# Optimization experiments

Hardware: AMD Instinct MI355X
Metric: run time of the kernel (lower is better)

## Reference

```python
import jax, jax.numpy as jnp
import numpy as np

B, T, I, H, OUT, L = 256, 1200, 16, 128, 1, 2


def _lstm_layer(x, W_ih, W_hh, b_ih, b_hh):
    # x: [B, T, Din]; W_ih: [4H, Din]; W_hh: [4H, H]
    # Precompute input contribution for all timesteps (one big GEMM),
    # then scan only the recurrent part.
    pre = jnp.einsum('btd,gd->btg', x, W_ih) + b_ih + b_hh  # [B, T, 4H]
    pre = jnp.swapaxes(pre, 0, 1)  # [T, B, 4H]
    h0 = jnp.zeros((x.shape[0], W_hh.shape[1]), dtype=x.dtype)
    c0 = jnp.zeros_like(h0)

    def step(carry, p_t):
        h, c = carry
        g = p_t + h @ W_hh.T  # [B, 4H]
        i, f, gg, o = jnp.split(g, 4, axis=-1)  # torch gate order: i, f, g, o
        i = jax.nn.sigmoid(i)
        f = jax.nn.sigmoid(f)
        gg = jnp.tanh(gg)
        o = jax.nn.sigmoid(o)
        c = f * c + i * gg
        h = o * jnp.tanh(c)
        return (h, c), h

    (_, _), hs = jax.lax.scan(step, (h0, c0), pre)  # hs: [T, B, H]
    return jnp.swapaxes(hs, 0, 1)  # [B, T, H]


def setup_inputs() -> dict:
    key = jax.random.key(0)
    ks = jax.random.split(key, 12)
    s = 0.08  # small init scale to keep gates unsaturated
    inp = {
        'x': jax.random.normal(ks[0], (B, T, I), dtype=jnp.float32),
        'W_ih0': jax.random.normal(ks[1], (4 * H, I), dtype=jnp.float32) * s,
        'W_hh0': jax.random.normal(ks[2], (4 * H, H), dtype=jnp.float32) * s,
        'b_ih0': jax.random.normal(ks[3], (4 * H,), dtype=jnp.float32) * s,
        'b_hh0': jax.random.normal(ks[4], (4 * H,), dtype=jnp.float32) * s,
        'W_ih1': jax.random.normal(ks[5], (4 * H, H), dtype=jnp.float32) * s,
        'W_hh1': jax.random.normal(ks[6], (4 * H, H), dtype=jnp.float32) * s,
        'b_ih1': jax.random.normal(ks[7], (4 * H,), dtype=jnp.float32) * s,
        'b_hh1': jax.random.normal(ks[8], (4 * H,), dtype=jnp.float32) * s,
        'W_lin': jax.random.normal(ks[9], (OUT, H), dtype=jnp.float32) * s,
        'b_lin': jax.random.normal(ks[10], (OUT,), dtype=jnp.float32) * s,
    }
    return inp


def reference(x, W_ih0, W_hh0, b_ih0, b_hh0, W_ih1, W_hh1, b_ih1, b_hh1, W_lin, b_lin):
    h1 = _lstm_layer(x, W_ih0, W_hh0, b_ih0, b_hh0)   # [B, T, H]
    h2 = _lstm_layer(h1, W_ih1, W_hh1, b_ih1, b_hh1)  # [B, T, H]
    out = jax.nn.relu(h2)
    out = jnp.einsum('bth,oh->bto', out, W_lin) + b_lin  # [B, T, OUT]
    return out.reshape(-1, 12)  # [B*T*OUT/12, 12]
```

## Files before the change

kernel.cpp:

```cpp
#include <hip/hip_runtime.h>
#include <hip/hip_fp16.h>

#define B_ 256
#define T_ 1200
#define I_ 16
#define H_ 128

typedef __attribute__((ext_vector_type(2))) _Float16 h2;
typedef __attribute__((ext_vector_type(8))) _Float16 f16x8;

#if __has_builtin(__builtin_amdgcn_fdot2)
__device__ __forceinline__ float fdot2(h2 a, h2 b, float c) {
  return __builtin_amdgcn_fdot2(a, b, c, false);
}
#else
__device__ __forceinline__ float fdot2(h2 a, h2 b, float c) {
  return fmaf((float)a.x, (float)b.x, fmaf((float)a.y, (float)b.y, c));
}
#endif

__device__ __forceinline__ float qsum(float x) {
  x += __int_as_float(__builtin_amdgcn_update_dpp(0, __float_as_int(x), 0xB1, 0xF, 0xF, true));
  x += __int_as_float(__builtin_amdgcn_update_dpp(0, __float_as_int(x), 0x4E, 0xF, 0xF, true));
  return x;
}

__device__ __forceinline__ float sigm(float x) {
  return __builtin_amdgcn_rcpf(1.f + __expf(-x));
}
__device__ __forceinline__ float tanh_(float x) {
  return 1.f - 2.f * __builtin_amdgcn_rcpf(1.f + __expf(2.f * x));
}

#define DECL16(p) h2 p##0,p##1,p##2,p##3,p##4,p##5,p##6,p##7,p##8,p##9,p##10,p##11,p##12,p##13,p##14,p##15;

#define LOADROW(p, src) { \
  const float4 v0_ = *(const float4*)((src) + 0); \
  const float4 v1_ = *(const float4*)((src) + 4); \
  const float4 v2_ = *(const float4*)((src) + 8); \
  const float4 v3_ = *(const float4*)((src) + 12); \
  const float4 v4_ = *(const float4*)((src) + 16); \
  const float4 v5_ = *(const float4*)((src) + 20); \
  const float4 v6_ = *(const float4*)((src) + 24); \
  const float4 v7_ = *(const float4*)((src) + 28); \
  p##0 .x=(_Float16)v0_.x;  p##0 .y=(_Float16)v0_.y;  p##1 .x=(_Float16)v0_.z;  p##1 .y=(_Float16)v0_.w; \
  p##2 .x=(_Float16)v1_.x;  p##2 .y=(_Float16)v1_.y;  p##3 .x=(_Float16)v1_.z;  p##3 .y=(_Float16)v1_.w; \
  p##4 .x=(_Float16)v2_.x;  p##4 .y=(_Float16)v2_.y;  p##5 .x=(_Float16)v2_.z;  p##5 .y=(_Float16)v2_.w; \
  p##6 .x=(_Float16)v3_.x;  p##6 .y=(_Float16)v3_.y;  p##7 .x=(_Float16)v3_.z;  p##7 .y=(_Float16)v3_.w; \
  p##8 .x=(_Float16)v4_.x;  p##8 .y=(_Float16)v4_.y;  p##9 .x=(_Float16)v4_.z;  p##9 .y=(_Float16)v4_.w; \
  p##10 .x=(_Float16)v5_.x; p##10 .y=(_Float16)v5_.y; p##11 .x=(_Float16)v5_.z; p##11 .y=(_Float16)v5_.w; \
  p##12 .x=(_Float16)v6_.x; p##12 .y=(_Float16)v6_.y; p##13 .x=(_Float16)v6_.z; p##13 .y=(_Float16)v6_.w; \
  p##14 .x=(_Float16)v7_.x; p##14 .y=(_Float16)v7_.y; p##15 .x=(_Float16)v7_.z; p##15 .y=(_Float16)v7_.w; }

#define H2AT(f, a, b) ({ h2 t_; t_.x = (f)[a]; t_.y = (f)[b]; t_; })

#define GDOT(mat, k0, k1, k2, k3, f) \
  a0 = fdot2(mat##_0_##k0, H2AT(f,0,1), a0); \
  a0 = fdot2(mat##_0_##k1, H2AT(f,2,3), a0); \
  a0 = fdot2(mat##_0_##k2, H2AT(f,4,5), a0); \
  a0 = fdot2(mat##_0_##k3, H2AT(f,6,7), a0); \
  a1 = fdot2(mat##_1_##k0, H2AT(f,0,1), a1); \
  a1 = fdot2(mat##_1_##k1, H2AT(f,2,3), a1); \
  a1 = fdot2(mat##_1_##k2, H2AT(f,4,5), a1); \
  a1 = fdot2(mat##_1_##k3, H2AT(f,6,7), a1); \
  a2 = fdot2(mat##_2_##k0, H2AT(f,0,1), a2); \
  a2 = fdot2(mat##_2_##k1, H2AT(f,2,3), a2); \
  a2 = fdot2(mat##_2_##k2, H2AT(f,4,5), a2); \
  a2 = fdot2(mat##_2_##k3, H2AT(f,6,7), a2); \
  a3 = fdot2(mat##_3_##k0, H2AT(f,0,1), a3); \
  a3 = fdot2(mat##_3_##k1, H2AT(f,2,3), a3); \
  a3 = fdot2(mat##_3_##k2, H2AT(f,4,5), a3); \
  a3 = fdot2(mat##_3_##k3, H2AT(f,6,7), a3);

#define MATDOT(mat, base) { \
  { const f16x8 f_ = *(const f16x8*)((base) + 0);  GDOT(mat, 0, 1, 2, 3,  f_) } \
  { const f16x8 f_ = *(const f16x8*)((base) + 8);  GDOT(mat, 4, 5, 6, 7,  f_) } \
  { const f16x8 f_ = *(const f16x8*)((base) + 16); GDOT(mat, 8, 9, 10,11, f_) } \
  { const f16x8 f_ = *(const f16x8*)((base) + 24); GDOT(mat, 12,13,14,15, f_) } }

__global__ __launch_bounds__(512)
__attribute__((amdgpu_waves_per_eu(2, 2)))
void lstm_fused(
    const float* __restrict__ xin,
    const float* __restrict__ Wih0, const float* __restrict__ Whh0,
    const float* __restrict__ bih0, const float* __restrict__ bhh0,
    const float* __restrict__ Wih1, const float* __restrict__ Whh1,
    const float* __restrict__ bih1, const float* __restrict__ bhh1,
    const float* __restrict__ Wlin, const float* __restrict__ blin,
    float* __restrict__ out)
{
  __shared__ __align__(16) __half buf0[2][H_];
  __shared__ __align__(16) __half buf1[2][H_];
  __shared__ __align__(16) float red[2][8];

  const int tid = threadIdx.x;
  const int c = tid & 3;
  const int j = tid >> 2;
  const int b = blockIdx.x;
  const int wv = tid >> 6;

  DECL16(w0_0_) DECL16(w0_1_) DECL16(w0_2_) DECL16(w0_3_)
  DECL16(wi_0_) DECL16(wi_1_) DECL16(wi_2_) DECL16(wi_3_)
  DECL16(wh_0_) DECL16(wh_1_) DECL16(wh_2_) DECL16(wh_3_)

  const int co = c * 32;
  LOADROW(w0_0_, Whh0 + (size_t)(0 * H_ + j) * H_ + co)
  LOADROW(w0_1_, Whh0 + (size_t)(1 * H_ + j) * H_ + co)
  LOADROW(w0_2_, Whh0 + (size_t)(2 * H_ + j) * H_ + co)
  LOADROW(w0_3_, Whh0 + (size_t)(3 * H_ + j) * H_ + co)
  LOADROW(wi_0_, Wih1 + (size_t)(0 * H_ + j) * H_ + co)
  LOADROW(wi_1_, Wih1 + (size_t)(1 * H_ + j) * H_ + co)
  LOADROW(wi_2_, Wih1 + (size_t)(2 * H_ + j) * H_ + co)
  LOADROW(wi_3_, Wih1 + (size_t)(3 * H_ + j) * H_ + co)
  LOADROW(wh_0_, Whh1 + (size_t)(0 * H_ + j) * H_ + co)
  LOADROW(wh_1_, Whh1 + (size_t)(1 * H_ + j) * H_ + co)
  LOADROW(wh_2_, Whh1 + (size_t)(2 * H_ + j) * H_ + co)
  LOADROW(wh_3_, Whh1 + (size_t)(3 * H_ + j) * H_ + co)

  h2 wx00, wx01, wx10, wx11, wx20, wx21, wx30, wx31;
  {
    const float4 v0 = *(const float4*)(Wih0 + (size_t)(0 * H_ + j) * I_ + 4 * c);
    const float4 v1 = *(const float4*)(Wih0 + (size_t)(1 * H_ + j) * I_ + 4 * c);
    const float4 v2 = *(const float4*)(Wih0 + (size_t)(2 * H_ + j) * I_ + 4 * c);
    const float4 v3 = *(const float4*)(Wih0 + (size_t)(3 * H_ + j) * I_ + 4 * c);
    wx00.x=(_Float16)v0.x; wx00.y=(_Float16)v0.y; wx01.x=(_Float16)v0.z; wx01.y=(_Float16)v0.w;
    wx10.x=(_Float16)v1.x; wx10.y=(_Float16)v1.y; wx11.x=(_Float16)v1.z; wx11.y=(_Float16)v1.w;
    wx20.x=(_Float16)v2.x; wx20.y=(_Float16)v2.y; wx21.x=(_Float16)v2.z; wx21.y=(_Float16)v2.w;
    wx30.x=(_Float16)v3.x; wx30.y=(_Float16)v3.y; wx31.x=(_Float16)v3.z; wx31.y=(_Float16)v3.w;
  }
  const float bs0_0 = bih0[0*H_+j] + bhh0[0*H_+j];
  const float bs0_1 = bih0[1*H_+j] + bhh0[1*H_+j];
  const float bs0_2 = bih0[2*H_+j] + bhh0[2*H_+j];
  const float bs0_3 = bih0[3*H_+j] + bhh0[3*H_+j];
  const float bs1_0 = bih1[0*H_+j] + bhh1[0*H_+j];
  const float bs1_1 = bih1[1*H_+j] + bhh1[1*H_+j];
  const float bs1_2 = bih1[2*H_+j] + bhh1[2*H_+j];
  const float bs1_3 = bih1[3*H_+j] + bhh1[3*H_+j];

  const float wl4 = Wlin[j] * 0.25f;
  const float bl = blin[0];

  if (tid < H_) {
    buf0[0][tid] = __float2half(0.f);
    buf1[0][tid] = __float2half(0.f);
  }
  float cst0 = 0.f, cst1 = 0.f;
  const float* xp = xin + (size_t)b * T_ * I_ + 4 * c;
  float* op = out + (size_t)b * T_;
  float4 xv_next = *(const float4*)xp;
  __syncthreads();

#pragma unroll 2
  for (int t = 0; t < T_; ++t) {
    const int rb = t & 1;
    const float4 xv = xv_next;
    xp += I_;
    if (t + 1 < T_) xv_next = *(const float4*)xp;
    float a0 = 0.f, a1 = 0.f, a2 = 0.f, a3 = 0.f;
    MATDOT(w0, &buf0[rb][co])
    {
      h2 xa, xb;
      xa.x = (_Float16)xv.x; xa.y = (_Float16)xv.y;
      xb.x = (_Float16)xv.z; xb.y = (_Float16)xv.w;
      a0 = fdot2(wx00, xa, fdot2(wx01, xb, a0));
      a1 = fdot2(wx10, xa, fdot2(wx11, xb, a1));
      a2 = fdot2(wx20, xa, fdot2(wx21, xb, a2));
      a3 = fdot2(wx30, xa, fdot2(wx31, xb, a3));
      const float g0 = qsum(a0) + bs0_0;
      const float g1 = qsum(a1) + bs0_1;
      const float g2 = qsum(a2) + bs0_2;
      const float g3 = qsum(a3) + bs0_3;
      const float ig = sigm(g0), fg = sigm(g1), gg = tanh_(g2), og = sigm(g3);
      cst0 = fg * cst0 + ig * gg;
      const float h0v = og * tanh_(cst0);
      if (c == 0) buf0[rb ^ 1][j] = __float2half(h0v);
    }
    __syncthreads();
    a0 = 0.f; a1 = 0.f; a2 = 0.f; a3 = 0.f;
    MATDOT(wi, &buf0[rb ^ 1][co])
    MATDOT(wh, &buf1[rb][co])
    const float g0 = qsum(a0) + bs1_0;
    const float g1 = qsum(a1) + bs1_1;
    const float g2 = qsum(a2) + bs1_2;
    const float g3 = qsum(a3) + bs1_3;
    const float ig = sigm(g0), fg = sigm(g1), gg = tanh_(g2), og = sigm(g3);
    cst1 = fg * cst1 + ig * gg;
    const float h1v = og * tanh_(cst1);
    if (c == 0) buf1[rb ^ 1][j] = __float2half(h1v);
    float val = fmaxf(h1v, 0.f) * wl4;
    val += __shfl_xor(val, 1);
    val += __shfl_xor(val, 2);
    val += __shfl_xor(val, 4);
    val += __shfl_xor(val, 8);
    val += __shfl_xor(val, 16);
    val += __shfl_xor(val, 32);
    if ((tid & 63) == 0) red[rb][wv] = val;
    __syncthreads();
    if (tid == ((t & 7) << 6)) {
      const float4 r0 = *(const float4*)(&red[rb][0]);
      const float4 r1 = *(const float4*)(&red[rb][4]);
      op[t] = bl + r0.x + r0.y + r0.z + r0.w + r1.x + r1.y + r1.z + r1.w;
    }
  }
}

extern "C" void kernel_launch(void* const* d_in, const int* in_sizes, int n_in,
                              void* d_out, int out_size, void* d_ws, size_t ws_size,
                              hipStream_t stream) {
  lstm_fused<<<B_, 512, 0, stream>>>(
      (const float*)d_in[0],
      (const float*)d_in[1], (const float*)d_in[2],
      (const float*)d_in[3], (const float*)d_in[4],
      (const float*)d_in[5], (const float*)d_in[6],
      (const float*)d_in[7], (const float*)d_in[8],
      (const float*)d_in[9], (const float*)d_in[10],
      (float*)d_out);
}
```

Measured before the change: 2.086 ms.

## Split each hidden unit across 8 lanes with 1024-thread blocks

Doubles the threads per block from 512 to 1024, so each hidden unit's dot product is split across 8 lanes instead of 4. Each lane now holds half as many fp16 weights in registers and does half the fdot2 work per step. The per-step reduction gains an extra ds_swizzle stage, and the final output reduction now combines 16 wave partials instead of 8. This shortens the serial per-timestep critical path, but makes each block-wide barrier more expensive and removes the waves_per_eu hint.

New measurement: 3.962 ms. 1.9x slower.

```diff
diff --git a/kernel.cpp b/kernel.cpp
--- a/kernel.cpp
+++ b/kernel.cpp
@@ -19,9 +19,10 @@
 }
 #endif
 
-__device__ __forceinline__ float qsum(float x) {
+__device__ __forceinline__ float osum(float x) {
   x += __int_as_float(__builtin_amdgcn_update_dpp(0, __float_as_int(x), 0xB1, 0xF, 0xF, true));
   x += __int_as_float(__builtin_amdgcn_update_dpp(0, __float_as_int(x), 0x4E, 0xF, 0xF, true));
+  x += __int_as_float(__builtin_amdgcn_ds_swizzle(__float_as_int(x), 0x101F));
   return x;
 }
 
@@ -32,25 +33,17 @@
   return 1.f - 2.f * __builtin_amdgcn_rcpf(1.f + __expf(2.f * x));
 }
 
-#define DECL16(p) h2 p##0,p##1,p##2,p##3,p##4,p##5,p##6,p##7,p##8,p##9,p##10,p##11,p##12,p##13,p##14,p##15;
-
-#define LOADROW(p, src) { \
+#define DECL8(p) h2 p##0,p##1,p##2,p##3,p##4,p##5,p##6,p##7;
+
+#define LOADROW8(p, src) { \
   const float4 v0_ = *(const float4*)((src) + 0); \
   const float4 v1_ = *(const float4*)((src) + 4); \
   const float4 v2_ = *(const float4*)((src) + 8); \
   const float4 v3_ = *(const float4*)((src) + 12); \
-  const float4 v4_ = *(const float4*)((src) + 16); \
-  const float4 v5_ = *(const float4*)((src) + 20); \
-  const float4 v6_ = *(const float4*)((src) + 24); \
-  const float4 v7_ = *(const float4*)((src) + 28); \
-  p##0 .x=(_Float16)v0_.x;  p##0 .y=(_Float16)v0_.y;  p##1 .x=(_Float16)v0_.z;  p##1 .y=(_Float16)v0_.w; \
-  p##2 .x=(_Float16)v1_.x;  p##2 .y=(_Float16)v1_.y;  p##3 .x=(_Float16)v1_.z;  p##3 .y=(_Float16)v1_.w; \
-  p##4 .x=(_Float16)v2_.x;  p##4 .y=(_Float16)v2_.y;  p##5 .x=(_Float16)v2_.z;  p##5 .y=(_Float16)v2_.w; \
-  p##6 .x=(_Float16)v3_.x;  p##6 .y=(_Float16)v3_.y;  p##7 .x=(_Float16)v3_.z;  p##7 .y=(_Float16)v3_.w; \
-  p##8 .x=(_Float16)v4_.x;  p##8 .y=(_Float16)v4_.y;  p##9 .x=(_Float16)v4_.z;  p##9 .y=(_Float16)v4_.w; \
-  p##10 .x=(_Float16)v5_.x; p##10 .y=(_Float16)v5_.y; p##11 .x=(_Float16)v5_.z; p##11 .y=(_Float16)v5_.w; \
-  p##12 .x=(_Float16)v6_.x; p##12 .y=(_Float16)v6_.y; p##13 .x=(_Float16)v6_.z; p##13 .y=(_Float16)v6_.w; \
-  p##14 .x=(_Float16)v7_.x; p##14 .y=(_Float16)v7_.y; p##15 .x=(_Float16)v7_.z; p##15 .y=(_Float16)v7_.w; }
+  p##0 .x=(_Float16)v0_.x; p##0 .y=(_Float16)v0_.y; p##1 .x=(_Float16)v0_.z; p##1 .y=(_Float16)v0_.w; \
+  p##2 .x=(_Float16)v1_.x; p##2 .y=(_Float16)v1_.y; p##3 .x=(_Float16)v1_.z; p##3 .y=(_Float16)v1_.w; \
+  p##4 .x=(_Float16)v2_.x; p##4 .y=(_Float16)v2_.y; p##5 .x=(_Float16)v2_.z; p##5 .y=(_Float16)v2_.w; \
+  p##6 .x=(_Float16)v3_.x; p##6 .y=(_Float16)v3_.y; p##7 .x=(_Float16)v3_.z; p##7 .y=(_Float16)v3_.w; }
 
 #define H2AT(f, a, b) ({ h2 t_; t_.x = (f)[a]; t_.y = (f)[b]; t_; })
 
@@ -72,15 +65,11 @@
   a3 = fdot2(mat##_3_##k2, H2AT(f,4,5), a3); \
   a3 = fdot2(mat##_3_##k3, H2AT(f,6,7), a3);
 
-#define MATDOT(mat, base) { \
-  { const f16x8 f_ = *(const f16x8*)((base) + 0);  GDOT(mat, 0, 1, 2, 3,  f_) } \
-  { const f16x8 f_ = *(const f16x8*)((base) + 8);  GDOT(mat, 4, 5, 6, 7,  f_) } \
-  { const f16x8 f_ = *(const f16x8*)((base) + 16); GDOT(mat, 8, 9, 10,11, f_) } \
-  { const f16x8 f_ = *(const f16x8*)((base) + 24); GDOT(mat, 12,13,14,15, f_) } }
-
-__global__ __launch_bounds__(512)
-__attribute__((amdgpu_waves_per_eu(2, 2)))
-void lstm_fused(
+#define MATDOT8(mat, base) { \
+  { const f16x8 f_ = *(const f16x8*)((base) + 0); GDOT(mat, 0, 1, 2, 3, f_) } \
+  { const f16x8 f_ = *(const f16x8*)((base) + 8); GDOT(mat, 4, 5, 6, 7, f_) } }
+
+__global__ __launch_bounds__(1024) void lstm_fused(
     const float* __restrict__ xin,
     const float* __restrict__ Wih0, const float* __restrict__ Whh0,
     const float* __restrict__ bih0, const float* __restrict__ bhh0,
@@ -91,42 +80,42 @@
 {
   __shared__ __align__(16) __half buf0[2][H_];
   __shared__ __align__(16) __half buf1[2][H_];
-  __shared__ __align__(16) float red[2][8];
+  __shared__ __align__(16) float red[2][16];
 
   const int tid = threadIdx.x;
-  const int c = tid & 3;
-  const int j = tid >> 2;
+  const int o = tid & 7;
+  const int j = tid >> 3;
   const int b = blockIdx.x;
   const int wv = tid >> 6;
 
-  DECL16(w0_0_) DECL16(w0_1_) DECL16(w0_2_) DECL16(w0_3_)
-  DECL16(wi_0_) DECL16(wi_1_) DECL16(wi_2_) DECL16(wi_3_)
-  DECL16(wh_0_) DECL16(wh_1_) DECL16(wh_2_) DECL16(wh_3_)
-
-  const int co = c * 32;
-  LOADROW(w0_0_, Whh0 + (size_t)(0 * H_ + j) * H_ + co)
-  LOADROW(w0_1_, Whh0 + (size_t)(1 * H_ + j) * H_ + co)
-  LOADROW(w0_2_, Whh0 + (size_t)(2 * H_ + j) * H_ + co)
-  LOADROW(w0_3_, Whh0 + (size_t)(3 * H_ + j) * H_ + co)
-  LOADROW(wi_0_, Wih1 + (size_t)(0 * H_ + j) * H_ + co)
-  LOADROW(wi_1_, Wih1 + (size_t)(1 * H_ + j) * H_ + co)
-  LOADROW(wi_2_, Wih1 + (size_t)(2 * H_ + j) * H_ + co)
-  LOADROW(wi_3_, Wih1 + (size_t)(3 * H_ + j) * H_ + co)
-  LOADROW(wh_0_, Whh1 + (size_t)(0 * H_ + j) * H_ + co)
-  LOADROW(wh_1_, Whh1 + (size_t)(1 * H_ + j) * H_ + co)
-  LOADROW(wh_2_, Whh1 + (size_t)(2 * H_ + j) * H_ + co)
-  LOADROW(wh_3_, Whh1 + (size_t)(3 * H_ + j) * H_ + co)
-
-  h2 wx00, wx01, wx10, wx11, wx20, wx21, wx30, wx31;
+  DECL8(w0_0_) DECL8(w0_1_) DECL8(w0_2_) DECL8(w0_3_)
+  DECL8(wi_0_) DECL8(wi_1_) DECL8(wi_2_) DECL8(wi_3_)
+  DECL8(wh_0_) DECL8(wh_1_) DECL8(wh_2_) DECL8(wh_3_)
+
+  const int co = o * 16;
+  LOADROW8(w0_0_, Whh0 + (size_t)(0 * H_ + j) * H_ + co)
+  LOADROW8(w0_1_, Whh0 + (size_t)(1 * H_ + j) * H_ + co)
+  LOADROW8(w0_2_, Whh0 + (size_t)(2 * H_ + j) * H_ + co)
+  LOADROW8(w0_3_, Whh0 + (size_t)(3 * H_ + j) * H_ + co)
+  LOADROW8(wi_0_, Wih1 + (size_t)(0 * H_ + j) * H_ + co)
+  LOADROW8(wi_1_, Wih1 + (size_t)(1 * H_ + j) * H_ + co)
+  LOADROW8(wi_2_, Wih1 + (size_t)(2 * H_ + j) * H_ + co)
+  LOADROW8(wi_3_, Wih1 + (size_t)(3 * H_ + j) * H_ + co)
+  LOADROW8(wh_0_, Whh1 + (size_t)(0 * H_ + j) * H_ + co)
+  LOADROW8(wh_1_, Whh1 + (size_t)(1 * H_ + j) * H_ + co)
+  LOADROW8(wh_2_, Whh1 + (size_t)(2 * H_ + j) * H_ + co)
+  LOADROW8(wh_3_, Whh1 + (size_t)(3 * H_ + j) * H_ + co)
+
+  h2 wx0, wx1, wx2, wx3;
   {
-    const float4 v0 = *(const float4*)(Wih0 + (size_t)(0 * H_ + j) * I_ + 4 * c);
-    const float4 v1 = *(const float4*)(Wih0 + (size_t)(1 * H_ + j) * I_ + 4 * c);
-    const float4 v2 = *(const float4*)(Wih0 + (size_t)(2 * H_ + j) * I_ + 4 * c);
-    const float4 v3 = *(const float4*)(Wih0 + (size_t)(3 * H_ + j) * I_ + 4 * c);
-    wx00.x=(_Float16)v0.x; wx00.y=(_Float16)v0.y; wx01.x=(_Float16)v0.z; wx01.y=(_Float16)v0.w;
-    wx10.x=(_Float16)v1.x; wx10.y=(_Float16)v1.y; wx11.x=(_Float16)v1.z; wx11.y=(_Float16)v1.w;
-    wx20.x=(_Float16)v2.x; wx20.y=(_Float16)v2.y; wx21.x=(_Float16)v2.z; wx21.y=(_Float16)v2.w;
-    wx30.x=(_Float16)v3.x; wx30.y=(_Float16)v3.y; wx31.x=(_Float16)v3.z; wx31.y=(_Float16)v3.w;
+    const float2 v0 = *(const float2*)(Wih0 + (size_t)(0 * H_ + j) * I_ + 2 * o);
+    const float2 v1 = *(const float2*)(Wih0 + (size_t)(1 * H_ + j) * I_ + 2 * o);
+    const float2 v2 = *(const float2*)(Wih0 + (size_t)(2 * H_ + j) * I_ + 2 * o);
+    const float2 v3 = *(const float2*)(Wih0 + (size_t)(3 * H_ + j) * I_ + 2 * o);
+    wx0.x=(_Float16)v0.x; wx0.y=(_Float16)v0.y;
+    wx1.x=(_Float16)v1.x; wx1.y=(_Float16)v1.y;
+    wx2.x=(_Float16)v2.x; wx2.y=(_Float16)v2.y;
+    wx3.x=(_Float16)v3.x; wx3.y=(_Float16)v3.y;
   }
   const float bs0_0 = bih0[0*H_+j] + bhh0[0*H_+j];
   const float bs0_1 = bih0[1*H_+j] + bhh0[1*H_+j];
@@ -137,7 +126,7 @@
   const float bs1_2 = bih1[2*H_+j] + bhh1[2*H_+j];
   const float bs1_3 = bih1[3*H_+j] + bhh1[3*H_+j];
 
-  const float wl4 = Wlin[j] * 0.25f;
+  const float wl8 = Wlin[j] * 0.125f;
   const float bl = blin[0];
 
   if (tid < H_) {
@@ -145,49 +134,48 @@
     buf1[0][tid] = __float2half(0.f);
   }
   float cst0 = 0.f, cst1 = 0.f;
-  const float* xp = xin + (size_t)b * T_ * I_ + 4 * c;
+  const float* xp = xin + (size_t)b * T_ * I_ + 2 * o;
   float* op = out + (size_t)b * T_;
-  float4 xv_next = *(const float4*)xp;
+  float2 xv_next = *(const float2*)xp;
   __syncthreads();
 
 #pragma unroll 2
   for (int t = 0; t < T_; ++t) {
     const int rb = t & 1;
-    const float4 xv = xv_next;
+    const float2 xv = xv_next;
     xp += I_;
-    if (t + 1 < T_) xv_next = *(const float4*)xp;
+    if (t + 1 < T_) xv_next = *(const float2*)xp;
     float a0 = 0.f, a1 = 0.f, a2 = 0.f, a3 = 0.f;
-    MATDOT(w0, &buf0[rb][co])
+    MATDOT8(w0, &buf0[rb][co])
     {
-      h2 xa, xb;
+      h2 xa;
       xa.x = (_Float16)xv.x; xa.y = (_Float16)xv.y;
-      xb.x = (_Float16)xv.z; xb.y = (_Float16)xv.w;
-      a0 = fdot2(wx00, xa, fdot2(wx01, xb, a0));
-      a1 = fdot2(wx10, xa, fdot2(wx11, xb, a1));
-      a2 = fdot2(wx20, xa, fdot2(wx21, xb, a2));
-      a3 = fdot2(wx30, xa, fdot2(wx31, xb, a3));
-      const float g0 = qsum(a0) + bs0_0;
-      const float g1 = qsum(a1) + bs0_1;
-      const float g2 = qsum(a2) + bs0_2;
-      const float g3 = qsum(a3) + bs0_3;
+      a0 = fdot2(wx0, xa, a0);
+      a1 = fdot2(wx1, xa, a1);
+      a2 = fdot2(wx2, xa, a2);
+      a3 = fdot2(wx3, xa, a3);
+      const float g0 = osum(a0) + bs0_0;
+      const float g1 = osum(a1) + bs0_1;
+      const float g2 = osum(a2) + bs0_2;
+      const float g3 = osum(a3) + bs0_3;
       const float ig = sigm(g0), fg = sigm(g1), gg = tanh_(g2), og = sigm(g3);
       cst0 = fg * cst0 + ig * gg;
       const float h0v = og * tanh_(cst0);
-      if (c == 0) buf0[rb ^ 1][j] = __float2half(h0v);
+      if (o == 0) buf0[rb ^ 1][j] = __float2half(h0v);
     }
     __syncthreads();
     a0 = 0.f; a1 = 0.f; a2 = 0.f; a3 = 0.f;
-    MATDOT(wi, &buf0[rb ^ 1][co])
-    MATDOT(wh, &buf1[rb][co])
-    const float g0 = qsum(a0) + bs1_0;
-    const float g1 = qsum(a1) + bs1_1;
-    const float g2 = qsum(a2) + bs1_2;
-    const float g3 = qsum(a3) + bs1_3;
+    MATDOT8(wi, &buf0[rb ^ 1][co])
+    MATDOT8(wh, &buf1[rb][co])
+    const float g0 = osum(a0) + bs1_0;
+    const float g1 = osum(a1) + bs1_1;
+    const float g2 = osum(a2) + bs1_2;
+    const float g3 = osum(a3) + bs1_3;
     const float ig = sigm(g0), fg = sigm(g1), gg = tanh_(g2), og = sigm(g3);
     cst1 = fg * cst1 + ig * gg;
     const float h1v = og * tanh_(cst1);
-    if (c == 0) buf1[rb ^ 1][j] = __float2half(h1v);
-    float val = fmaxf(h1v, 0.f) * wl4;
+    if (o == 0) buf1[rb ^ 1][j] = __float2half(h1v);
+    float val = fmaxf(h1v, 0.f) * wl8;
     val += __shfl_xor(val, 1);
     val += __shfl_xor(val, 2);
     val += __shfl_xor(val, 4);
@@ -196,10 +184,13 @@
     val += __shfl_xor(val, 32);
     if ((tid & 63) == 0) red[rb][wv] = val;
     __syncthreads();
-    if (tid == ((t & 7) << 6)) {
+    if (tid == ((t & 15) << 6)) {
       const float4 r0 = *(const float4*)(&red[rb][0]);
       const float4 r1 = *(const float4*)(&red[rb][4]);
-      op[t] = bl + r0.x + r0.y + r0.z + r0.w + r1.x + r1.y + r1.z + r1.w;
+      const float4 r2 = *(const float4*)(&red[rb][8]);
+      const float4 r3 = *(const float4*)(&red[rb][12]);
+      op[t] = bl + r0.x + r0.y + r0.z + r0.w + r1.x + r1.y + r1.z + r1.w
+                 + r2.x + r2.y + r2.z + r2.w + r3.x + r3.y + r3.z + r3.w;
     }
   }
 }
@@ -207,7 +198,7 @@
 extern "C" void kernel_launch(void* const* d_in, const int* in_sizes, int n_in,
                               void* d_out, int out_size, void* d_ws, size_t ws_size,
                               hipStream_t stream) {
-  lstm_fused<<<B_, 512, 0, stream>>>(
+  lstm_fused<<<B_, 1024, 0, stream>>>(
       (const float*)d_in[0],
       (const float*)d_in[1], (const float*)d_in[2],
       (const float*)d_in[3], (const float*)d_in[4],
```
